# Kernel tuning notes

Hardware: AMD Instinct MI355X
Metric: run time of the kernel (lower is better)

The kernel has to match this reference:

```python
import jax, jax.numpy as jnp
import numpy as np

N_EMBED = 1024
HEAD_COUNT = 16
HEAD_SIZE = 64  # HEAD_COUNT * HEAD_SIZE == N_EMBED
SEQ = 2048
BATCH = 2


def setup_inputs() -> dict:
    key = jax.random.key(0)
    k_ix, k_q, k_k, k_v, k_p, k_b = jax.random.split(key, 6)
    scale = 1.0 / np.sqrt(N_EMBED)
    inp = {
        "ix": jax.random.normal(k_ix, (BATCH, SEQ, N_EMBED), dtype=jnp.float32),
        # per-head projection weights, stored as x @ W form: [H, C, D]
        "Wq": jax.random.normal(k_q, (HEAD_COUNT, N_EMBED, HEAD_SIZE), dtype=jnp.float32) * scale,
        "Wk": jax.random.normal(k_k, (HEAD_COUNT, N_EMBED, HEAD_SIZE), dtype=jnp.float32) * scale,
        "Wv": jax.random.normal(k_v, (HEAD_COUNT, N_EMBED, HEAD_SIZE), dtype=jnp.float32) * scale,
        # output projection (Linear with bias): y = x @ Wp + bp
        "Wp": jax.random.normal(k_p, (N_EMBED, N_EMBED), dtype=jnp.float32) * scale,
        "bp": jax.random.normal(k_b, (N_EMBED,), dtype=jnp.float32) * scale,
    }
    return inp


def reference(ix, Wq, Wk, Wv, Wp, bp):
    B, T, C = ix.shape
    # per-head projections: [B, H, T, D]
    Q = jnp.einsum("btc,hcd->bhtd", ix, Wq)
    K = jnp.einsum("btc,hcd->bhtd", ix, Wk)
    V = jnp.einsum("btc,hcd->bhtd", ix, Wv)
    # NOTE: faithful to source -- scores are MULTIPLIED by sqrt(C) (C = n_embed)
    scores = jnp.einsum("bhtd,bhsd->bhts", Q, K) * (C ** 0.5)
    causal = jnp.tril(jnp.ones((T, T), dtype=bool))
    scores = jnp.where(causal, scores, -jnp.inf)
    wei = jax.nn.softmax(scores, axis=-1)
    out = jnp.einsum("bhts,bhsd->bhtd", wei, V)
    # concat heads (matches torch.cat over per-head outputs along last dim)
    out = out.transpose(0, 2, 1, 3).reshape(B, T, -1)
    return out @ Wp + bp
```

## Files before the change

kernel.cpp:

```cpp
#include <hip/hip_runtime.h>

#define BATCH 2
#define SEQL  2048
#define NEMB  1024
#define NH    16
#define HD    64
#define MROWS (BATCH*SEQL)

#define QSCALE 46.166241308446828f

typedef short bf16x8 __attribute__((ext_vector_type(8)));
typedef float f32x16 __attribute__((ext_vector_type(16)));

__device__ __forceinline__ unsigned short f2bf(float x) {
    union { float f; unsigned u; } v; v.f = x;
    unsigned r = v.u + 0x7FFFu + ((v.u >> 16) & 1u);
    return (unsigned short)(r >> 16);
}
__device__ __forceinline__ void split_bf16(float x, unsigned short& hi, unsigned short& lo) {
    hi = f2bf(x);
    union { unsigned u; float f; } h; h.u = ((unsigned)hi) << 16;
    lo = f2bf(x - h.f);
}
__device__ __forceinline__ float bf2f(unsigned short b) {
    union { unsigned u; float f; } v; v.u = ((unsigned)b) << 16;
    return v.f;
}
__device__ __forceinline__ unsigned cvt_pk_bf16(float a, float b) {
    unsigned r;
    asm("v_cvt_pk_bf16_f32 %0, %1, %2" : "=v"(r) : "v"(a), "v"(b));
    return r;
}
__device__ __forceinline__ void plane_swap(unsigned& a, unsigned& b) {
    asm volatile("v_permlane32_swap_b32 %0, %1" : "+v"(a), "+v"(b));
}

__device__ __forceinline__ int slot16(int chunk, int lane) {
    return chunk * 66 + (lane & 31) + 33 * (lane >> 5);
}

__global__ __launch_bounds__(256) void convert_kernel(
    const float* __restrict__ ixsrc,
    const float* __restrict__ Wq, const float* __restrict__ Wk,
    const float* __restrict__ Wv, const float* __restrict__ Wp,
    unsigned short* __restrict__ ixhi, unsigned short* __restrict__ ixlo,
    unsigned short* __restrict__ qhi, unsigned short* __restrict__ qlo,
    unsigned short* __restrict__ khi, unsigned short* __restrict__ klo,
    unsigned short* __restrict__ vhi, unsigned short* __restrict__ pt)
{
    __shared__ float tile[64][68];
    const int bid = blockIdx.x;
    const int tid = threadIdx.x;

    if (bid < 4096) {
        int i = (bid * 256 + tid) * 4;
        float4 v = *(const float4*)(ixsrc + i);
        unsigned short h[4], l[4];
        split_bf16(v.x, h[0], l[0]); split_bf16(v.y, h[1], l[1]);
        split_bf16(v.z, h[2], l[2]); split_bf16(v.w, h[3], l[3]);
        uint2 ph, pl;
        ph.x = h[0] | ((unsigned)h[1] << 16); ph.y = h[2] | ((unsigned)h[3] << 16);
        pl.x = l[0] | ((unsigned)l[1] << 16); pl.y = l[2] | ((unsigned)l[3] << 16);
        *(uint2*)(ixhi + i) = ph;
        *(uint2*)(ixlo + i) = pl;
        return;
    }

    const int t  = bid - 4096;
    const int z  = t >> 8;
    const int rem = t & 255;
    const int hb = (rem >> 4) & 15;
    const int c0 = (rem & 15) * 64;
    const float* src; int rstride; unsigned short* dhi; unsigned short* dlo;
    if (z == 0)      { src = Wq + (size_t)hb * 65536; rstride = 64;   dhi = qhi; dlo = qlo; }
    else if (z == 1) { src = Wk + (size_t)hb * 65536; rstride = 64;   dhi = khi; dlo = klo; }
    else if (z == 2) { src = Wv + (size_t)hb * 65536; rstride = 64;   dhi = vhi; dlo = nullptr; }
    else             { src = Wp + (size_t)hb * 64;    rstride = 1024; dhi = pt;  dlo = nullptr; }
    #pragma unroll
    for (int i = 0; i < 4; ++i) {
        int fidx = i * 256 + tid;
        int r  = fidx >> 4;
        int dq = (fidx & 15) * 4;
        float4 v = *(const float4*)(src + (size_t)(c0 + r) * rstride + dq);
        *(float4*)&tile[r][dq] = v;
    }
    __syncthreads();
    #pragma unroll
    for (int i = 0; i < 4; ++i) {
        int fidx = i * 256 + tid;
        int d  = fidx >> 4;
        int cq = (fidx & 15) * 4;
        size_t base = (size_t)(hb * 64 + d) * 1024 + c0 + cq;
        unsigned short hh[4], ll[4];
        #pragma unroll
        for (int j = 0; j < 4; ++j) split_bf16(tile[cq + j][d], hh[j], ll[j]);
        uint2 ph; ph.x = hh[0] | ((unsigned)hh[1] << 16); ph.y = hh[2] | ((unsigned)hh[3] << 16);
        *(uint2*)(dhi + base) = ph;
        if (dlo) {
            uint2 pl; pl.x = ll[0] | ((unsigned)ll[1] << 16); pl.y = ll[2] | ((unsigned)ll[3] << 16);
            *(uint2*)(dlo + base) = pl;
        }
    }
}

__global__ __launch_bounds__(256, 2) void qkv_gemm(
    const unsigned short* __restrict__ Ahi, const unsigned short* __restrict__ Alo,
    const unsigned short* __restrict__ Bq_hi, const unsigned short* __restrict__ Bq_lo,
    const unsigned short* __restrict__ Bk_hi, const unsigned short* __restrict__ Bk_lo,
    const unsigned short* __restrict__ Bv_hi,
    unsigned short* __restrict__ Qhi, unsigned short* __restrict__ Qlo,
    unsigned short* __restrict__ Khi, unsigned short* __restrict__ Klo,
    unsigned short* __restrict__ Vt)
{
    __shared__ unsigned short smem[2][4][4224];

    const int bid = blockIdx.x;
    const int tid  = threadIdx.x;
    const int wid  = tid >> 6, lane = tid & 63;
    const int wr   = wid >> 1, wc = wid & 1;

    if (bid < 512) {
        const int z   = bid >> 8;
        const int xy  = bid & 255;
        const int m0  = (xy & 31) * 128;
        const int n0  = (xy >> 5) * 128;
        const unsigned short* __restrict__ Bhi = z ? Bk_hi : Bq_hi;
        const unsigned short* __restrict__ Blo = z ? Bk_lo : Bq_lo;
        unsigned short* __restrict__ Ohi = z ? Khi : Qhi;
        unsigned short* __restrict__ Olo = z ? Klo : Qlo;
        const float oscale = z ? 1.0f : QSCALE;

        int roff_[2], slot_[2];
        #pragma unroll
        for (int q = 0; q < 2; ++q) {
            int f   = q * 256 + tid;
            int row = f >> 2;
            int k8  = (f & 3) * 8;
            roff_[q] = row * 1024 + k8;
            slot_[q] = slot16((row >> 5) * 2 + (k8 >> 4), (row & 31) + 32 * ((k8 >> 3) & 1)) * 8;
        }
        const unsigned short* __restrict__ Ah = Ahi + (size_t)m0 * 1024;
        const unsigned short* __restrict__ Bh = Bhi + (size_t)n0 * 1024;
        const unsigned short* __restrict__ Al = Alo + (size_t)m0 * 1024;
        const unsigned short* __restrict__ Bl = Blo + (size_t)n0 * 1024;

        bf16x8 pah[2], pbh[2], pal[2], pbl[2];

        #define LOADT(KK)  do { _Pragma("unroll")                               \
            for (int q = 0; q < 2; ++q) {                                       \
                pah[q] = *(const bf16x8*)(Ah + roff_[q] + (KK));                \
                pbh[q] = *(const bf16x8*)(Bh + roff_[q] + (KK));                \
                pal[q] = *(const bf16x8*)(Al + roff_[q] + (KK));                \
                pbl[q] = *(const bf16x8*)(Bl + roff_[q] + (KK));                \
            } } while (0)

        #define WRITET(NB) do { _Pragma("unroll")                               \
            for (int q = 0; q < 2; ++q) {                                       \
                *(bf16x8*)(&smem[NB][0][slot_[q]]) = pah[q];                    \
                *(bf16x8*)(&smem[NB][1][slot_[q]]) = pbh[q];                    \
                *(bf16x8*)(&smem[NB][2][slot_[q]]) = pal[q];                    \
                *(bf16x8*)(&smem[NB][3][slot_[q]]) = pbl[q];                    \
            } } while (0)

        f32x16 acc[2][2] = {};

        LOADT(0);
        WRITET(0);
        LOADT(32);

        for (int t = 0; t < 32; ++t) {
            __syncthreads();
            if (t + 1 < 32) {
                WRITET((t + 1) & 1);
                if (t + 2 < 32) LOADT((t + 2) * 32);
            }
            const int cb = t & 1;
            const unsigned short* a_hi = smem[cb][0];
            const unsigned short* b_hi = smem[cb][1];
            const unsigned short* a_lo = smem[cb][2];
            const unsigned short* b_lo = smem[cb][3];

            #pragma unroll
            for (int kch = 0; kch < 2; ++kch) {
                bf16x8 ah[2], bh_[2], al[2], bl[2];
                #pragma unroll
                for (int mt = 0; mt < 2; ++mt) {
                    ah[mt] = *(const bf16x8*)(a_hi + slot16((2 * wr + mt) * 2 + kch, lane) * 8);
                    al[mt] = *(const bf16x8*)(a_lo + slot16((2 * wr + mt) * 2 + kch, lane) * 8);
                }
                #pragma unroll
                for (int nt = 0; nt < 2; ++nt) {
                    bh_[nt] = *(const bf16x8*)(b_hi + slot16((2 * wc + nt) * 2 + kch, lane) * 8);
                    bl[nt]  = *(const bf16x8*)(b_lo + slot16((2 * wc + nt) * 2 + kch, lane) * 8);
                }
                #pragma unroll
                for (int mt = 0; mt < 2; ++mt)
                    #pragma unroll
                    for (int nt = 0; nt < 2; ++nt) {
                        acc[mt][nt] = __builtin_amdgcn_mfma_f32_32x32x16_bf16(ah[mt], bh_[nt], acc[mt][nt], 0, 0, 0);
                        acc[mt][nt] = __builtin_amdgcn_mfma_f32_32x32x16_bf16(ah[mt], bl[nt],  acc[mt][nt], 0, 0, 0);
                        acc[mt][nt] = __builtin_amdgcn_mfma_f32_32x32x16_bf16(al[mt], bh_[nt], acc[mt][nt], 0, 0, 0);
                    }
            }
        }
        #undef LOADT
        #undef WRITET

        #pragma unroll
        for (int mt = 0; mt < 2; ++mt) {
            #pragma unroll
            for (int nt = 0; nt < 2; ++nt) {
                const int ncol = n0 + wc * 64 + nt * 32 + (lane & 31);
                const int head = ncol >> 6, d = ncol & 63;
                #pragma unroll
                for (int r = 0; r < 16; ++r) {
                    int mrow = m0 + wr * 64 + mt * 32 + (r & 3) + 8 * (r >> 2) + 4 * (lane >> 5);
                    int bb = mrow >> 11, tt = mrow & (SEQL - 1);
                    size_t idx = ((size_t)(bb * NH + head) * SEQL + tt) * HD + d;
                    float v = acc[mt][nt][r] * oscale;
                    unsigned short hi = f2bf(v);
                    Ohi[idx] = hi;
                    union { unsigned u; float f; } hf; hf.u = ((unsigned)hi) << 16;
                    Olo[idx] = f2bf(v - hf.f);
                }
            }
        }
    } else {
        const int vid = bid - 512;
        const int m0  = (vid >> 4) * 128;
        const int n0  = (vid & 15) * 64;

        int roffA_[2], slotA_[2], roffB, slotB;
        #pragma unroll
        for (int q = 0; q < 2; ++q) {
            int f   = q * 256 + tid;
            int row = f >> 2;
            int k8  = (f & 3) * 8;
            roffA_[q] = row * 1024 + k8;
            slotA_[q] = slot16((row >> 5) * 2 + (k8 >> 4), (row & 31) + 32 * ((k8 >> 3) & 1)) * 8;
        }
        {
            int row = tid >> 2;
            int k8  = (tid & 3) * 8;
            roffB  = row * 1024 + k8;
            slotB  = slot16((row >> 5) * 2 + (k8 >> 4), (row & 31) + 32 * ((k8 >> 3) & 1)) * 8;
        }
        const unsigned short* __restrict__ Ah = Ahi + (size_t)m0 * 1024;
        const unsigned short* __restrict__ Bh = Bv_hi + (size_t)n0 * 1024;

        bf16x8 pa[2], pb;
        #pragma unroll
        for (int q = 0; q < 2; ++q) pa[q] = *(const bf16x8*)(Ah + roffA_[q]);
        pb = *(const bf16x8*)(Bh + roffB);
        #pragma unroll
        for (int q = 0; q < 2; ++q) *(bf16x8*)(&smem[0][0][slotA_[q]]) = pa[q];
        *(bf16x8*)(&smem[0][1][slotB]) = pb;
        #pragma unroll
        for (int q = 0; q < 2; ++q) pa[q] = *(const bf16x8*)(Ah + roffA_[q] + 32);
        pb = *(const bf16x8*)(Bh + roffB + 32);

        f32x16 acc[2] = {};

        for (int t = 0; t < 32; ++t) {
            __syncthreads();
            if (t + 1 < 32) {
                const int nb = (t + 1) & 1;
                #pragma unroll
                for (int q = 0; q < 2; ++q) *(bf16x8*)(&smem[nb][0][slotA_[q]]) = pa[q];
                *(bf16x8*)(&smem[nb][1][slotB]) = pb;
                if (t + 2 < 32) {
                    #pragma unroll
                    for (int q = 0; q < 2; ++q) pa[q] = *(const bf16x8*)(Ah + roffA_[q] + (t + 2) * 32);
                    pb = *(const bf16x8*)(Bh + roffB + (t + 2) * 32);
                }
            }
            const int cb = t & 1;
            const unsigned short* a_s = smem[cb][0];
            const unsigned short* b_s = smem[cb][1];
            #pragma unroll
            for (int kch = 0; kch < 2; ++kch) {
                bf16x8 ah[2], bh_;
                #pragma unroll
                for (int mt = 0; mt < 2; ++mt)
                    ah[mt] = *(const bf16x8*)(a_s + slot16((2 * wr + mt) * 2 + kch, lane) * 8);
                bh_ = *(const bf16x8*)(b_s + slot16(wc * 2 + kch, lane) * 8);
                #pragma unroll
                for (int mt = 0; mt < 2; ++mt)
                    acc[mt] = __builtin_amdgcn_mfma_f32_32x32x16_bf16(bh_, ah[mt], acc[mt], 0, 0, 0);
            }
        }

        #pragma unroll
        for (int mt = 0; mt < 2; ++mt) {
            const int mcol = m0 + wr * 64 + mt * 32 + (lane & 31);
            const int bb = mcol >> 11, tt = mcol & (SEQL - 1);
            #pragma unroll
            for (int r = 0; r < 16; ++r) {
                int nrow = n0 + wc * 32 + (r & 3) + 8 * (r >> 2) + 4 * (lane >> 5);
                int head = nrow >> 6, dd = nrow & 63;
                Vt[((size_t)(bb * NH + head) * HD + dd) * SEQL + tt] = f2bf(acc[mt][r]);
            }
        }
    }
}

__global__ __launch_bounds__(256) void attn_mfma_kernel(
    const unsigned short* __restrict__ Qhi, const unsigned short* __restrict__ Qlo,
    const unsigned short* __restrict__ Khi, const unsigned short* __restrict__ Klo,
    const unsigned short* __restrict__ Vt,
    unsigned short* __restrict__ Op0, unsigned short* __restrict__ Op1,
    float* __restrict__ Ml)
{
    __shared__ unsigned short smem[2][3][4224];

    const int bid  = blockIdx.x;
    const int xcd  = bid & 7;
    const int idx  = bid >> 3;
    const int bh   = xcd * 4 + (idx & 3);
    const int rest = idx >> 2;
    const int j    = 15 - (rest >> 1);
    const int sp   = rest & 1;

    const int tid  = threadIdx.x;
    const int wid  = tid >> 6;
    const int lane = tid & 63;
    const int ln   = lane & 31;
    const int h    = lane >> 5;

    const int qb_idx = 4 * j + wid;
    const int qb     = qb_idx * 32;
    const int qglob  = qb + ln;
    const int cutoff = 2 * j + (wid >> 1);
    const int tbeg   = sp ? (j + 1) : 0;
    const int tend   = sp ? (2 * j + 2) : (j + 1);

    const unsigned short* __restrict__ Qbh = Qhi + (size_t)bh * SEQL * HD;
    const unsigned short* __restrict__ Qbl = Qlo + (size_t)bh * SEQL * HD;
    const unsigned short* __restrict__ Kbh = Khi + (size_t)bh * SEQL * HD;
    const unsigned short* __restrict__ Kbl = Klo + (size_t)bh * SEQL * HD;
    const unsigned short* __restrict__ Vtb = Vt  + (size_t)bh * HD * SEQL;

    bf16x8 qhi[4], qlo[4];
    #pragma unroll
    for (int c = 0; c < 4; ++c) {
        qhi[c] = *(const bf16x8*)(Qbh + (size_t)qglob * HD + c * 16 + h * 8);
        qlo[c] = *(const bf16x8*)(Qbl + (size_t)qglob * HD + c * 16 + h * 8);
    }

    int s_[2], d8_[2], ks_[2];
    #pragma unroll
    for (int ff = 0; ff < 2; ++ff) {
        int fidx = ff * 256 + tid;
        s_[ff]  = fidx >> 3;
        d8_[ff] = fidx & 7;
        ks_[ff] = slot16((s_[ff] >> 5) * 4 + (d8_[ff] >> 1),
                         (s_[ff] & 31) + 32 * (d8_[ff] & 1)) * 8;
    }

    bf16x8 kh[2], kl[2], vv[2];
    {
        const int s0p = tbeg * 64;
        #pragma unroll
        for (int ff = 0; ff < 2; ++ff) {
            kh[ff] = *(const bf16x8*)(Kbh + (size_t)(s0p + s_[ff]) * HD + d8_[ff] * 8);
            kl[ff] = *(const bf16x8*)(Kbl + (size_t)(s0p + s_[ff]) * HD + d8_[ff] * 8);
            vv[ff] = *(const bf16x8*)(Vtb + (size_t)s_[ff] * SEQL + s0p + d8_[ff] * 8);
        }
        const int pb = tbeg & 1;
        #pragma unroll
        for (int ff = 0; ff < 2; ++ff) {
            *(bf16x8*)(&smem[pb][0][ks_[ff]]) = kh[ff];
            *(bf16x8*)(&smem[pb][1][ks_[ff]]) = kl[ff];
            *(bf16x8*)(&smem[pb][2][ks_[ff]]) = vv[ff];
        }
        if (tbeg + 1 < tend) {
            const int s0n = (tbeg + 1) * 64;
            #pragma unroll
            for (int ff = 0; ff < 2; ++ff) {
                kh[ff] = *(const bf16x8*)(Kbh + (size_t)(s0n + s_[ff]) * HD + d8_[ff] * 8);
                kl[ff] = *(const bf16x8*)(Kbl + (size_t)(s0n + s_[ff]) * HD + d8_[ff] * 8);
                vv[ff] = *(const bf16x8*)(Vtb + (size_t)s_[ff] * SEQL + s0n + d8_[ff] * 8);
            }
        }
    }

    f32x16 oacc[2] = {};
    float m_run = -1e30f, l_run = 0.f;

    for (int t = tbeg; t < tend; ++t) {
        __syncthreads();
        if (t + 1 < tend) {
            const int nb = (t + 1) & 1;
            #pragma unroll
            for (int ff = 0; ff < 2; ++ff) {
                *(bf16x8*)(&smem[nb][0][ks_[ff]]) = kh[ff];
                *(bf16x8*)(&smem[nb][1][ks_[ff]]) = kl[ff];
                *(bf16x8*)(&smem[nb][2][ks_[ff]]) = vv[ff];
            }
            if (t + 2 < tend) {
                const int s0n = (t + 2) * 64;
                #pragma unroll
                for (int ff = 0; ff < 2; ++ff) {
                    kh[ff] = *(const bf16x8*)(Kbh + (size_t)(s0n + s_[ff]) * HD + d8_[ff] * 8);
                    kl[ff] = *(const bf16x8*)(Kbl + (size_t)(s0n + s_[ff]) * HD + d8_[ff] * 8);
                    vv[ff] = *(const bf16x8*)(Vtb + (size_t)s_[ff] * SEQL + s0n + d8_[ff] * 8);
                }
            }
        }

        if (t <= cutoff) {
            const int cb = t & 1;
            const int s0 = t * 64;
            const bf16x8* khf = (const bf16x8*)&smem[cb][0][0];
            const bf16x8* klf = (const bf16x8*)&smem[cb][1][0];
            const bf16x8* vtf = (const bf16x8*)&smem[cb][2][0];

            f32x16 sacc[2] = {};
            __builtin_amdgcn_s_setprio(1);
            #pragma unroll
            for (int sb = 0; sb < 2; ++sb) {
                #pragma unroll
                for (int c = 0; c < 4; ++c) {
                    bf16x8 ah = khf[slot16(sb * 4 + c, lane)];
                    bf16x8 al = klf[slot16(sb * 4 + c, lane)];
                    sacc[sb] = __builtin_amdgcn_mfma_f32_32x32x16_bf16(ah, qhi[c], sacc[sb], 0, 0, 0);
                    sacc[sb] = __builtin_amdgcn_mfma_f32_32x32x16_bf16(ah, qlo[c], sacc[sb], 0, 0, 0);
                    sacc[sb] = __builtin_amdgcn_mfma_f32_32x32x16_bf16(al, qhi[c], sacc[sb], 0, 0, 0);
                }
            }
            __builtin_amdgcn_s_setprio(0);

            if ((s0 + 63) > qb) {
                #pragma unroll
                for (int sb = 0; sb < 2; ++sb)
                    #pragma unroll
                    for (int r = 0; r < 16; ++r) {
                        int srow = (r & 3) + 8 * (r >> 2) + 4 * h + sb * 32;
                        if ((s0 + srow) > qglob) sacc[sb][r] = -1e30f;
                    }
            }

            float mtile = -1e30f;
            #pragma unroll
            for (int sb = 0; sb < 2; ++sb)
                #pragma unroll
                for (int r = 0; r < 16; ++r)
                    mtile = fmaxf(mtile, sacc[sb][r]);
            mtile = fmaxf(mtile, __shfl_xor(mtile, 32));

            if (!__all(mtile - m_run <= 11.5f)) {
                const float mnew  = fmaxf(m_run, mtile);
                const float alpha = exp2f(m_run - mnew);
                l_run *= alpha;
                #pragma unroll
                for (int dt = 0; dt < 2; ++dt)
                    #pragma unroll
                    for (int r = 0; r < 16; ++r)
                        oacc[dt][r] *= alpha;
                m_run = mnew;
            }

            float ps0 = 0.f, ps1 = 0.f;
            unsigned pw[2][8];
            #pragma unroll
            for (int sb = 0; sb < 2; ++sb) {
                #pragma unroll
                for (int r2 = 0; r2 < 8; ++r2) {
                    float p0 = exp2f(sacc[sb][2 * r2]     - m_run);
                    float p1 = exp2f(sacc[sb][2 * r2 + 1] - m_run);
                    if (sb == 0) ps0 += p0 + p1; else ps1 += p0 + p1;
                    pw[sb][r2] = cvt_pk_bf16(p0, p1);
                }
            }
            float psum = ps0 + ps1;
            psum += __shfl_xor(psum, 32);
            l_run += psum;

            bf16x8 pfrag[4];
            #pragma unroll
            for (int sb = 0; sb < 2; ++sb) {
                #pragma unroll
                for (int c = 0; c < 2; ++c) {
                    unsigned u0 = pw[sb][4 * c + 0], u2 = pw[sb][4 * c + 2];
                    unsigned u1 = pw[sb][4 * c + 1], u3 = pw[sb][4 * c + 3];
                    plane_swap(u0, u2);
                    plane_swap(u1, u3);
                    union { unsigned u[4]; bf16x8 v; } cvt;
                    cvt.u[0] = u0; cvt.u[1] = u1; cvt.u[2] = u2; cvt.u[3] = u3;
                    pfrag[sb * 2 + c] = cvt.v;
                }
            }

            __builtin_amdgcn_s_setprio(1);
            #pragma unroll
            for (int dt = 0; dt < 2; ++dt)
                #pragma unroll
                for (int sc = 0; sc < 4; ++sc)
                    oacc[dt] = __builtin_amdgcn_mfma_f32_32x32x16_bf16(
                        vtf[slot16(dt * 4 + sc, lane)], pfrag[sc], oacc[dt], 0, 0, 0);
            __builtin_amdgcn_s_setprio(0);
        }
    }

    unsigned short* op = (sp ? Op1 : Op0)
        + ((size_t)(bh >> 4) * SEQL + qglob) * NEMB + (bh & 15) * HD;
    #pragma unroll
    for (int dt = 0; dt < 2; ++dt) {
        #pragma unroll
        for (int rg = 0; rg < 4; ++rg) {
            int d0 = dt * 32 + rg * 8 + h * 4;
            uint2 w;
            w.x = cvt_pk_bf16(oacc[dt][rg * 4 + 0], oacc[dt][rg * 4 + 1]);
            w.y = cvt_pk_bf16(oacc[dt][rg * 4 + 2], oacc[dt][rg * 4 + 3]);
            *(uint2*)(op + d0) = w;
        }
    }
    if (h == 0) {
        float2 mlv; mlv.x = m_run; mlv.y = l_run;
        *(float2*)(Ml + ((size_t)(sp * 32 + bh) * SEQL + qglob) * 2) = mlv;
    }
}

__global__ __launch_bounds__(256) void attn_merge_kernel(
    unsigned short* __restrict__ Op0, const unsigned short* __restrict__ Op1,
    const float* __restrict__ Ml)
{
    const int gid  = blockIdx.x * 256 + threadIdx.x;
    const int row  = gid >> 7;
    const int col  = (gid & 127) * 8;
    const int bh   = ((row >> 11) << 4) + (col >> 6);
    const int q    = row & (SEQL - 1);

    float2 ml0 = *(const float2*)(Ml + ((size_t)bh * SEQL + q) * 2);
    float2 ml1 = *(const float2*)(Ml + ((size_t)(32 + bh) * SEQL + q) * 2);
    const float M  = fmaxf(ml0.x, ml1.x);
    const float w0 = exp2f(ml0.x - M);
    const float w1 = exp2f(ml1.x - M);
    const float rd = 1.0f / (ml0.y * w0 + ml1.y * w1);
    const float f0 = w0 * rd, f1 = w1 * rd;

    size_t off = (size_t)row * NEMB + col;
    uint4 a = *(const uint4*)(Op0 + off);
    uint4 b = *(const uint4*)(Op1 + off);
    const unsigned short* ap = (const unsigned short*)&a;
    const unsigned short* bp = (const unsigned short*)&b;
    uint4 o;
    unsigned* opw = (unsigned*)&o;
    #pragma unroll
    for (int i = 0; i < 4; ++i) {
        float r0 = bf2f(ap[2*i])     * f0 + bf2f(bp[2*i])     * f1;
        float r1 = bf2f(ap[2*i + 1]) * f0 + bf2f(bp[2*i + 1]) * f1;
        opw[i] = cvt_pk_bf16(r0, r1);
    }
    *(uint4*)(Op0 + off) = o;
}

__global__ __launch_bounds__(256, 2) void out_proj_kernel(
    const unsigned short* __restrict__ A, const unsigned short* __restrict__ B,
    const float* __restrict__ bias, float* __restrict__ out)
{
    __shared__ unsigned short smem[2][2][4224];

    const int m0 = blockIdx.x * 128;
    const int n0 = blockIdx.y * 128;
    const int tid  = threadIdx.x;
    const int wid  = tid >> 6, lane = tid & 63;
    const int wr   = wid >> 1, wc = wid & 1;

    int roff_[2], slot_[2];
    #pragma unroll
    for (int q = 0; q < 2; ++q) {
        int f   = q * 256 + tid;
        int row = f >> 2;
        int k8  = (f & 3) * 8;
        roff_[q] = row * 1024 + k8;
        slot_[q] = slot16((row >> 5) * 2 + (k8 >> 4), (row & 31) + 32 * ((k8 >> 3) & 1)) * 8;
    }
    const unsigned short* __restrict__ Ab = A + (size_t)m0 * 1024;
    const unsigned short* __restrict__ Bb = B + (size_t)n0 * 1024;

    bf16x8 pa[2], pb[2];
    #pragma unroll
    for (int q = 0; q < 2; ++q) {
        pa[q] = *(const bf16x8*)(Ab + roff_[q]);
        pb[q] = *(const bf16x8*)(Bb + roff_[q]);
    }
    #pragma unroll
    for (int q = 0; q < 2; ++q) {
        *(bf16x8*)(&smem[0][0][slot_[q]]) = pa[q];
        *(bf16x8*)(&smem[0][1][slot_[q]]) = pb[q];
    }
    #pragma unroll
    for (int q = 0; q < 2; ++q) {
        pa[q] = *(const bf16x8*)(Ab + roff_[q] + 32);
        pb[q] = *(const bf16x8*)(Bb + roff_[q] + 32);
    }

    f32x16 acc[2][2] = {};

    for (int t = 0; t < 32; ++t) {
        __syncthreads();
        if (t + 1 < 32) {
            const int nb = (t + 1) & 1;
            #pragma unroll
            for (int q = 0; q < 2; ++q) {
                *(bf16x8*)(&smem[nb][0][slot_[q]]) = pa[q];
                *(bf16x8*)(&smem[nb][1][slot_[q]]) = pb[q];
            }
            if (t + 2 < 32) {
                #pragma unroll
                for (int q = 0; q < 2; ++q) {
                    pa[q] = *(const bf16x8*)(Ab + roff_[q] + (t + 2) * 32);
                    pb[q] = *(const bf16x8*)(Bb + roff_[q] + (t + 2) * 32);
                }
            }
        }
        const int cb = t & 1;
        const unsigned short* a_s = smem[cb][0];
        const unsigned short* b_s = smem[cb][1];
        #pragma unroll
        for (int kch = 0; kch < 2; ++kch) {
            bf16x8 ah[2], bh_[2];
            #pragma unroll
            for (int mt = 0; mt < 2; ++mt)
                ah[mt] = *(const bf16x8*)(a_s + slot16((2 * wr + mt) * 2 + kch, lane) * 8);
            #pragma unroll
            for (int nt = 0; nt < 2; ++nt)
                bh_[nt] = *(const bf16x8*)(b_s + slot16((2 * wc + nt) * 2 + kch, lane) * 8);
            #pragma unroll
            for (int mt = 0; mt < 2; ++mt)
                #pragma unroll
                for (int nt = 0; nt < 2; ++nt)
                    acc[mt][nt] = __builtin_amdgcn_mfma_f32_32x32x16_bf16(ah[mt], bh_[nt], acc[mt][nt], 0, 0, 0);
        }
    }

    #pragma unroll
    for (int mt = 0; mt < 2; ++mt) {
        #pragma unroll
        for (int nt = 0; nt < 2; ++nt) {
            const int ncol = n0 + wc * 64 + nt * 32 + (lane & 31);
            const float bv = bias[ncol];
            #pragma unroll
            for (int r = 0; r < 16; ++r) {
                int mrow = m0 + wr * 64 + mt * 32 + (r & 3) + 8 * (r >> 2) + 4 * (lane >> 5);
                out[(size_t)mrow * 1024 + ncol] = acc[mt][nt][r] + bv;
            }
        }
    }
}

extern "C" void kernel_launch(void* const* d_in, const int* in_sizes, int n_in,
                              void* d_out, int out_size, void* d_ws, size_t ws_size,
                              hipStream_t stream)
{
    const float* ix = (const float*)d_in[0];
    const float* Wq = (const float*)d_in[1];
    const float* Wk = (const float*)d_in[2];
    const float* Wv = (const float*)d_in[3];
    const float* Wp = (const float*)d_in[4];
    const float* bp = (const float*)d_in[5];
    float* out = (float*)d_out;

    char* ws = (char*)d_ws;
    #define WSOFF(mb) ((unsigned short*)(ws + (size_t)(mb) * 1024 * 1024))
    unsigned short* ix_hi  = WSOFF(0);
    unsigned short* ix_lo  = WSOFF(8);
    unsigned short* Wqt_hi = WSOFF(16);
    unsigned short* Wqt_lo = WSOFF(18);
    unsigned short* Wkt_hi = WSOFF(20);
    unsigned short* Wkt_lo = WSOFF(22);
    unsigned short* Wvt_hi = WSOFF(24);
    unsigned short* Qhi    = WSOFF(26);
    unsigned short* Qlo    = WSOFF(34);
    unsigned short* Khi    = WSOFF(42);
    unsigned short* Klo    = WSOFF(50);
    unsigned short* Wpt    = WSOFF(58);
    unsigned short* Op0    = WSOFF(0);
    unsigned short* Op1    = WSOFF(8);
    float*          Ml     = (float*)WSOFF(16);
    unsigned short* Vt     = (unsigned short*)d_out;
    #undef WSOFF

    convert_kernel<<<5120, 256, 0, stream>>>(
        ix, Wq, Wk, Wv, Wp, ix_hi, ix_lo,
        Wqt_hi, Wqt_lo, Wkt_hi, Wkt_lo, Wvt_hi, Wpt);
    qkv_gemm<<<1024, 256, 0, stream>>>(
        ix_hi, ix_lo, Wqt_hi, Wqt_lo, Wkt_hi, Wkt_lo, Wvt_hi,
        Qhi, Qlo, Khi, Klo, Vt);
    attn_mfma_kernel<<<1024, 256, 0, stream>>>(Qhi, Qlo, Khi, Klo, Vt, Op0, Op1, Ml);
    attn_merge_kernel<<<MROWS * NEMB / 8 / 256, 256, 0, stream>>>(Op0, Op1, Ml);
    out_proj_kernel<<<dim3(MROWS / 128, NEMB / 128), 256, 0, stream>>>(Op0, Wpt, bp, out);
}
```

Measured before the change: 173.2 us.

## Fuse ix bf16 split into QKV GEMM and attention merge into out-proj

Removes the separate pass that converts ix into hi/lo bf16 planes. The QKV GEMM now loads fp32 ix directly and splits it to hi/lo bf16 in registers. The separate attention merge kernel is also removed. The out-projection kernel now reads both partial outputs plus their max/sum stats and combines them while loading its A tiles. This cuts two kernel launches and the intermediate global writes and reads, in exchange for double-width fp32 A loads and redundant conversion and merge arithmetic, since each A tile is reloaded by every N-block.

```diff
diff --git a/kernel.cpp b/kernel.cpp
--- a/kernel.cpp
+++ b/kernel.cpp
@@ -34,43 +34,38 @@
 __device__ __forceinline__ void plane_swap(unsigned& a, unsigned& b) {
     asm volatile("v_permlane32_swap_b32 %0, %1" : "+v"(a), "+v"(b));
 }
+__device__ __forceinline__ void split8(const float4& f0, const float4& f1,
+                                       bf16x8& hi8, bf16x8& lo8) {
+    const float* f = (const float*)&f0;
+    float tmp[8] = { f0.x, f0.y, f0.z, f0.w, f1.x, f1.y, f1.z, f1.w };
+    #pragma unroll
+    for (int j = 0; j < 8; ++j) {
+        unsigned short h, l;
+        split_bf16(tmp[j], h, l);
+        hi8[j] = (short)h;
+        lo8[j] = (short)l;
+    }
+    (void)f;
+}
 
 __device__ __forceinline__ int slot16(int chunk, int lane) {
     return chunk * 66 + (lane & 31) + 33 * (lane >> 5);
 }
 
 __global__ __launch_bounds__(256) void convert_kernel(
-    const float* __restrict__ ixsrc,
     const float* __restrict__ Wq, const float* __restrict__ Wk,
     const float* __restrict__ Wv, const float* __restrict__ Wp,
-    unsigned short* __restrict__ ixhi, unsigned short* __restrict__ ixlo,
     unsigned short* __restrict__ qhi, unsigned short* __restrict__ qlo,
     unsigned short* __restrict__ khi, unsigned short* __restrict__ klo,
     unsigned short* __restrict__ vhi, unsigned short* __restrict__ pt)
 {
     __shared__ float tile[64][68];
-    const int bid = blockIdx.x;
-    const int tid = threadIdx.x;
-
-    if (bid < 4096) {
-        int i = (bid * 256 + tid) * 4;
-        float4 v = *(const float4*)(ixsrc + i);
-        unsigned short h[4], l[4];
-        split_bf16(v.x, h[0], l[0]); split_bf16(v.y, h[1], l[1]);
-        split_bf16(v.z, h[2], l[2]); split_bf16(v.w, h[3], l[3]);
-        uint2 ph, pl;
-        ph.x = h[0] | ((unsigned)h[1] << 16); ph.y = h[2] | ((unsigned)h[3] << 16);
-        pl.x = l[0] | ((unsigned)l[1] << 16); pl.y = l[2] | ((unsigned)l[3] << 16);
-        *(uint2*)(ixhi + i) = ph;
-        *(uint2*)(ixlo + i) = pl;
-        return;
-    }
-
-    const int t  = bid - 4096;
+    const int t  = blockIdx.x;
     const int z  = t >> 8;
     const int rem = t & 255;
     const int hb = (rem >> 4) & 15;
     const int c0 = (rem & 15) * 64;
+    const int tid = threadIdx.x;
     const float* src; int rstride; unsigned short* dhi; unsigned short* dlo;
     if (z == 0)      { src = Wq + (size_t)hb * 65536; rstride = 64;   dhi = qhi; dlo = qlo; }
     else if (z == 1) { src = Wk + (size_t)hb * 65536; rstride = 64;   dhi = khi; dlo = klo; }
@@ -104,7 +99,7 @@
 }
 
 __global__ __launch_bounds__(256, 2) void qkv_gemm(
-    const unsigned short* __restrict__ Ahi, const unsigned short* __restrict__ Alo,
+    const float* __restrict__ ix,
     const unsigned short* __restrict__ Bq_hi, const unsigned short* __restrict__ Bq_lo,
     const unsigned short* __restrict__ Bk_hi, const unsigned short* __restrict__ Bk_lo,
     const unsigned short* __restrict__ Bv_hi,
@@ -139,18 +134,18 @@
             roff_[q] = row * 1024 + k8;
             slot_[q] = slot16((row >> 5) * 2 + (k8 >> 4), (row & 31) + 32 * ((k8 >> 3) & 1)) * 8;
         }
-        const unsigned short* __restrict__ Ah = Ahi + (size_t)m0 * 1024;
+        const float* __restrict__ Axf = ix + (size_t)m0 * 1024;
         const unsigned short* __restrict__ Bh = Bhi + (size_t)n0 * 1024;
-        const unsigned short* __restrict__ Al = Alo + (size_t)m0 * 1024;
         const unsigned short* __restrict__ Bl = Blo + (size_t)n0 * 1024;
 
         bf16x8 pah[2], pbh[2], pal[2], pbl[2];
 
         #define LOADT(KK)  do { _Pragma("unroll")                               \
             for (int q = 0; q < 2; ++q) {                                       \
-                pah[q] = *(const bf16x8*)(Ah + roff_[q] + (KK));                \
+                float4 f0 = *(const float4*)(Axf + roff_[q] + (KK));            \
+                float4 f1 = *(const float4*)(Axf + roff_[q] + (KK) + 4);        \
+                split8(f0, f1, pah[q], pal[q]);                                 \
                 pbh[q] = *(const bf16x8*)(Bh + roff_[q] + (KK));                \
-                pal[q] = *(const bf16x8*)(Al + roff_[q] + (KK));                \
                 pbl[q] = *(const bf16x8*)(Bl + roff_[q] + (KK));                \
             } } while (0)
 
@@ -245,18 +240,30 @@
             roffB  = row * 1024 + k8;
             slotB  = slot16((row >> 5) * 2 + (k8 >> 4), (row & 31) + 32 * ((k8 >> 3) & 1)) * 8;
         }
-        const unsigned short* __restrict__ Ah = Ahi + (size_t)m0 * 1024;
+        const float* __restrict__ Axf = ix + (size_t)m0 * 1024;
         const unsigned short* __restrict__ Bh = Bv_hi + (size_t)n0 * 1024;
 
         bf16x8 pa[2], pb;
         #pragma unroll
-        for (int q = 0; q < 2; ++q) pa[q] = *(const bf16x8*)(Ah + roffA_[q]);
+        for (int q = 0; q < 2; ++q) {
+            float4 f0 = *(const float4*)(Axf + roffA_[q]);
+            float4 f1 = *(const float4*)(Axf + roffA_[q] + 4);
+            float t8[8] = { f0.x, f0.y, f0.z, f0.w, f1.x, f1.y, f1.z, f1.w };
+            #pragma unroll
+            for (int j = 0; j < 8; ++j) pa[q][j] = (short)f2bf(t8[j]);
+        }
         pb = *(const bf16x8*)(Bh + roffB);
         #pragma unroll
         for (int q = 0; q < 2; ++q) *(bf16x8*)(&smem[0][0][slotA_[q]]) = pa[q];
         *(bf16x8*)(&smem[0][1][slotB]) = pb;
         #pragma unroll
-        for (int q = 0; q < 2; ++q) pa[q] = *(const bf16x8*)(Ah + roffA_[q] + 32);
+        for (int q = 0; q < 2; ++q) {
+            float4 f0 = *(const float4*)(Axf + roffA_[q] + 32);
+            float4 f1 = *(const float4*)(Axf + roffA_[q] + 36);
+            float t8[8] = { f0.x, f0.y, f0.z, f0.w, f1.x, f1.y, f1.z, f1.w };
+            #pragma unroll
+            for (int j = 0; j < 8; ++j) pa[q][j] = (short)f2bf(t8[j]);
+        }
         pb = *(const bf16x8*)(Bh + roffB + 32);
 
         f32x16 acc[2] = {};
@@ -270,7 +277,13 @@
                 *(bf16x8*)(&smem[nb][1][slotB]) = pb;
                 if (t + 2 < 32) {
                     #pragma unroll
-                    for (int q = 0; q < 2; ++q) pa[q] = *(const bf16x8*)(Ah + roffA_[q] + (t + 2) * 32);
+                    for (int q = 0; q < 2; ++q) {
+                        float4 f0 = *(const float4*)(Axf + roffA_[q] + (t + 2) * 32);
+                        float4 f1 = *(const float4*)(Axf + roffA_[q] + (t + 2) * 32 + 4);
+                        float t8[8] = { f0.x, f0.y, f0.z, f0.w, f1.x, f1.y, f1.z, f1.w };
+                        #pragma unroll
+                        for (int j = 0; j < 8; ++j) pa[q][j] = (short)f2bf(t8[j]);
+                    }
                     pb = *(const bf16x8*)(Bh + roffB + (t + 2) * 32);
                 }
             }
@@ -521,42 +534,10 @@
     }
 }
 
-__global__ __launch_bounds__(256) void attn_merge_kernel(
-    unsigned short* __restrict__ Op0, const unsigned short* __restrict__ Op1,
-    const float* __restrict__ Ml)
-{
-    const int gid  = blockIdx.x * 256 + threadIdx.x;
-    const int row  = gid >> 7;
-    const int col  = (gid & 127) * 8;
-    const int bh   = ((row >> 11) << 4) + (col >> 6);
-    const int q    = row & (SEQL - 1);
-
-    float2 ml0 = *(const float2*)(Ml + ((size_t)bh * SEQL + q) * 2);
-    float2 ml1 = *(const float2*)(Ml + ((size_t)(32 + bh) * SEQL + q) * 2);
-    const float M  = fmaxf(ml0.x, ml1.x);
-    const float w0 = exp2f(ml0.x - M);
-    const float w1 = exp2f(ml1.x - M);
-    const float rd = 1.0f / (ml0.y * w0 + ml1.y * w1);
-    const float f0 = w0 * rd, f1 = w1 * rd;
-
-    size_t off = (size_t)row * NEMB + col;
-    uint4 a = *(const uint4*)(Op0 + off);
-    uint4 b = *(const uint4*)(Op1 + off);
-    const unsigned short* ap = (const unsigned short*)&a;
-    const unsigned short* bp = (const unsigned short*)&b;
-    uint4 o;
-    unsigned* opw = (unsigned*)&o;
-    #pragma unroll
-    for (int i = 0; i < 4; ++i) {
-        float r0 = bf2f(ap[2*i])     * f0 + bf2f(bp[2*i])     * f1;
-        float r1 = bf2f(ap[2*i + 1]) * f0 + bf2f(bp[2*i + 1]) * f1;
-        opw[i] = cvt_pk_bf16(r0, r1);
-    }
-    *(uint4*)(Op0 + off) = o;
-}
-
 __global__ __launch_bounds__(256, 2) void out_proj_kernel(
-    const unsigned short* __restrict__ A, const unsigned short* __restrict__ B,
+    const unsigned short* __restrict__ Op0, const unsigned short* __restrict__ Op1,
+    const float* __restrict__ Ml,
+    const unsigned short* __restrict__ B,
     const float* __restrict__ bias, float* __restrict__ out)
 {
     __shared__ unsigned short smem[2][2][4224];
@@ -567,22 +548,49 @@
     const int wid  = tid >> 6, lane = tid & 63;
     const int wr   = wid >> 1, wc = wid & 1;
 
-    int roff_[2], slot_[2];
+    int roff_[2], slot_[2], k8_[2];
+    size_t mlbase_[2];
     #pragma unroll
     for (int q = 0; q < 2; ++q) {
         int f   = q * 256 + tid;
         int row = f >> 2;
         int k8  = (f & 3) * 8;
         roff_[q] = row * 1024 + k8;
+        k8_[q]   = k8;
         slot_[q] = slot16((row >> 5) * 2 + (k8 >> 4), (row & 31) + 32 * ((k8 >> 3) & 1)) * 8;
-    }
-    const unsigned short* __restrict__ Ab = A + (size_t)m0 * 1024;
+        const int mrow = m0 + row;
+        mlbase_[q] = ((size_t)(mrow >> 11) * 16 * SEQL + (mrow & (SEQL - 1))) * 2;
+    }
+    const size_t abase = (size_t)m0 * 1024;
     const unsigned short* __restrict__ Bb = B + (size_t)n0 * 1024;
 
+    #define LOADA(q, KK, dst) do {                                              \
+        const int col  = (KK) + k8_[q];                                         \
+        const int head = col >> 6;                                              \
+        const size_t mloff = mlbase_[q] + (size_t)head * (SEQL * 2);            \
+        float2 ml0 = *(const float2*)(Ml + mloff);                              \
+        float2 ml1 = *(const float2*)(Ml + mloff + 32 * SEQL * 2);              \
+        const float M  = fmaxf(ml0.x, ml1.x);                                   \
+        const float w0 = exp2f(ml0.x - M);                                      \
+        const float w1 = exp2f(ml1.x - M);                                      \
+        const float rd = 1.0f / (ml0.y * w0 + ml1.y * w1);                      \
+        const float f0 = w0 * rd, f1 = w1 * rd;                                 \
+        uint4 av = *(const uint4*)(Op0 + abase + roff_[q] + (KK));              \
+        uint4 bv = *(const uint4*)(Op1 + abase + roff_[q] + (KK));              \
+        const unsigned short* ap = (const unsigned short*)&av;                  \
+        const unsigned short* bp = (const unsigned short*)&bv;                  \
+        unsigned* dw = (unsigned*)&(dst);                                       \
+        _Pragma("unroll")                                                       \
+        for (int i_ = 0; i_ < 4; ++i_) {                                        \
+            float r0 = bf2f(ap[2*i_])   * f0 + bf2f(bp[2*i_])   * f1;           \
+            float r1 = bf2f(ap[2*i_+1]) * f0 + bf2f(bp[2*i_+1]) * f1;           \
+            dw[i_] = cvt_pk_bf16(r0, r1);                                       \
+        } } while (0)
+
     bf16x8 pa[2], pb[2];
     #pragma unroll
     for (int q = 0; q < 2; ++q) {
-        pa[q] = *(const bf16x8*)(Ab + roff_[q]);
+        LOADA(q, 0, pa[q]);
         pb[q] = *(const bf16x8*)(Bb + roff_[q]);
     }
     #pragma unroll
@@ -592,7 +600,7 @@
     }
     #pragma unroll
     for (int q = 0; q < 2; ++q) {
-        pa[q] = *(const bf16x8*)(Ab + roff_[q] + 32);
+        LOADA(q, 32, pa[q]);
         pb[q] = *(const bf16x8*)(Bb + roff_[q] + 32);
     }
 
@@ -610,7 +618,7 @@
             if (t + 2 < 32) {
                 #pragma unroll
                 for (int q = 0; q < 2; ++q) {
-                    pa[q] = *(const bf16x8*)(Ab + roff_[q] + (t + 2) * 32);
+                    LOADA(q, (t + 2) * 32, pa[q]);
                     pb[q] = *(const bf16x8*)(Bb + roff_[q] + (t + 2) * 32);
                 }
             }
@@ -634,6 +642,7 @@
                     acc[mt][nt] = __builtin_amdgcn_mfma_f32_32x32x16_bf16(ah[mt], bh_[nt], acc[mt][nt], 0, 0, 0);
         }
     }
+    #undef LOADA
 
     #pragma unroll
     for (int mt = 0; mt < 2; ++mt) {
@@ -664,8 +673,6 @@
 
     char* ws = (char*)d_ws;
     #define WSOFF(mb) ((unsigned short*)(ws + (size_t)(mb) * 1024 * 1024))
-    unsigned short* ix_hi  = WSOFF(0);
-    unsigned short* ix_lo  = WSOFF(8);
     unsigned short* Wqt_hi = WSOFF(16);
     unsigned short* Wqt_lo = WSOFF(18);
     unsigned short* Wkt_hi = WSOFF(20);
@@ -682,13 +689,12 @@
     unsigned short* Vt     = (unsigned short*)d_out;
     #undef WSOFF
 
-    convert_kernel<<<5120, 256, 0, stream>>>(
-        ix, Wq, Wk, Wv, Wp, ix_hi, ix_lo,
-        Wqt_hi, Wqt_lo, Wkt_hi, Wkt_lo, Wvt_hi, Wpt);
+    convert_kernel<<<1024, 256, 0, stream>>>(
+        Wq, Wk, Wv, Wp, Wqt_hi, Wqt_lo, Wkt_hi, Wkt_lo, Wvt_hi, Wpt);
     qkv_gemm<<<1024, 256, 0, stream>>>(
-        ix_hi, ix_lo, Wqt_hi, Wqt_lo, Wkt_hi, Wkt_lo, Wvt_hi,
+        ix, Wqt_hi, Wqt_lo, Wkt_hi, Wkt_lo, Wvt_hi,
         Qhi, Qlo, Khi, Klo, Vt);
     attn_mfma_kernel<<<1024, 256, 0, stream>>>(Qhi, Qlo, Khi, Klo, Vt, Op0, Op1, Ml);
-    attn_merge_kernel<<<MROWS * NEMB / 8 / 256, 256, 0, stream>>>(Op0, Op1, Ml);
-    out_proj_kernel<<<dim3(MROWS / 128, NEMB / 128), 256, 0, stream>>>(Op0, Wpt, bp, out);
-}
+    out_proj_kernel<<<dim3(MROWS / 128, NEMB / 128), 256, 0, stream>>>(
+        Op0, Op1, Ml, Wpt, bp, out);
+}
```

After: 189.3 us. 9.3% more time.

## Stage Q/K projection GEMM tiles via direct global-to-LDS loads

Applied to the files above, without the earlier changes.

The Q/K branch of the QKV projection kernel now copies its hi/lo A and B tiles straight from global memory into LDS with global_load_lds (16-byte lanes), instead of loading into registers and then writing to LDS. The shared layout becomes unpadded and fragment-major, so each wave's load lands exactly where the MFMA fragment reads expect it. The V branch is updated to index the flattened buffer. The aim is to cut VGPR staging, LDS write instructions and register pressure, and to overlap the next tile's fetch with MFMA work. In exchange it drops the padded bank-conflict-avoiding layout and relies on correct vmcnt waits before the barrier.

```diff
diff --git a/kernel.cpp b/kernel.cpp
--- a/kernel.cpp
+++ b/kernel.cpp
@@ -33,6 +33,9 @@
 }
 __device__ __forceinline__ void plane_swap(unsigned& a, unsigned& b) {
     asm volatile("v_permlane32_swap_b32 %0, %1" : "+v"(a), "+v"(b));
+}
+__device__ __forceinline__ void gload_lds16(const unsigned short* g, unsigned short* l) {
+    __builtin_amdgcn_global_load_lds((const unsigned int*)g, (unsigned int*)l, 16, 0, 0);
 }
 
 __device__ __forceinline__ int slot16(int chunk, int lane) {
@@ -112,7 +115,7 @@
     unsigned short* __restrict__ Khi, unsigned short* __restrict__ Klo,
     unsigned short* __restrict__ Vt)
 {
-    __shared__ unsigned short smem[2][4][4224];
+    __shared__ unsigned short smem[32768];
 
     const int bid = blockIdx.x;
     const int tid  = threadIdx.x;
@@ -130,68 +133,54 @@
         unsigned short* __restrict__ Olo = z ? Klo : Qlo;
         const float oscale = z ? 1.0f : QSCALE;
 
-        int roff_[2], slot_[2];
-        #pragma unroll
-        for (int q = 0; q < 2; ++q) {
-            int f   = q * 256 + tid;
-            int row = f >> 2;
-            int k8  = (f & 3) * 8;
-            roff_[q] = row * 1024 + k8;
-            slot_[q] = slot16((row >> 5) * 2 + (k8 >> 4), (row & 31) + 32 * ((k8 >> 3) & 1)) * 8;
-        }
         const unsigned short* __restrict__ Ah = Ahi + (size_t)m0 * 1024;
         const unsigned short* __restrict__ Bh = Bhi + (size_t)n0 * 1024;
         const unsigned short* __restrict__ Al = Alo + (size_t)m0 * 1024;
         const unsigned short* __restrict__ Bl = Blo + (size_t)n0 * 1024;
 
-        bf16x8 pah[2], pbh[2], pal[2], pbl[2];
-
-        #define LOADT(KK)  do { _Pragma("unroll")                               \
-            for (int q = 0; q < 2; ++q) {                                       \
-                pah[q] = *(const bf16x8*)(Ah + roff_[q] + (KK));                \
-                pbh[q] = *(const bf16x8*)(Bh + roff_[q] + (KK));                \
-                pal[q] = *(const bf16x8*)(Al + roff_[q] + (KK));                \
-                pbl[q] = *(const bf16x8*)(Bl + roff_[q] + (KK));                \
-            } } while (0)
-
-        #define WRITET(NB) do { _Pragma("unroll")                               \
-            for (int q = 0; q < 2; ++q) {                                       \
-                *(bf16x8*)(&smem[NB][0][slot_[q]]) = pah[q];                    \
-                *(bf16x8*)(&smem[NB][1][slot_[q]]) = pbh[q];                    \
-                *(bf16x8*)(&smem[NB][2][slot_[q]]) = pal[q];                    \
-                *(bf16x8*)(&smem[NB][3][slot_[q]]) = pbl[q];                    \
-            } } while (0)
+        const size_t goff = (size_t)(wid * 32 + (lane & 31)) * 1024 + (lane >> 5) * 8;
+        const int cb0 = wid * 2 * 512;
+
+        #define ISSUE(KK, NB) do {                                              \
+            unsigned short* lb = smem + (NB) * 16384 + cb0;                     \
+            gload_lds16(Ah + goff + (KK),      lb + 0 * 4096);                  \
+            gload_lds16(Ah + goff + (KK) + 16, lb + 0 * 4096 + 512);            \
+            gload_lds16(Bh + goff + (KK),      lb + 1 * 4096);                  \
+            gload_lds16(Bh + goff + (KK) + 16, lb + 1 * 4096 + 512);            \
+            gload_lds16(Al + goff + (KK),      lb + 2 * 4096);                  \
+            gload_lds16(Al + goff + (KK) + 16, lb + 2 * 4096 + 512);            \
+            gload_lds16(Bl + goff + (KK),      lb + 3 * 4096);                  \
+            gload_lds16(Bl + goff + (KK) + 16, lb + 3 * 4096 + 512);            \
+        } while (0)
 
         f32x16 acc[2][2] = {};
 
-        LOADT(0);
-        WRITET(0);
-        LOADT(32);
+        ISSUE(0, 0);
 
         for (int t = 0; t < 32; ++t) {
             __syncthreads();
-            if (t + 1 < 32) {
-                WRITET((t + 1) & 1);
-                if (t + 2 < 32) LOADT((t + 2) * 32);
-            }
-            const int cb = t & 1;
-            const unsigned short* a_hi = smem[cb][0];
-            const unsigned short* b_hi = smem[cb][1];
-            const unsigned short* a_lo = smem[cb][2];
-            const unsigned short* b_lo = smem[cb][3];
+            if (t + 1 < 32) ISSUE((t + 1) * 32, (t + 1) & 1);
+
+            const unsigned short* base = smem + (t & 1) * 16384;
+            const unsigned short* a_hi = base;
+            const unsigned short* b_hi = base + 4096;
+            const unsigned short* a_lo = base + 8192;
+            const unsigned short* b_lo = base + 12288;
 
             #pragma unroll
             for (int kch = 0; kch < 2; ++kch) {
                 bf16x8 ah[2], bh_[2], al[2], bl[2];
                 #pragma unroll
                 for (int mt = 0; mt < 2; ++mt) {
-                    ah[mt] = *(const bf16x8*)(a_hi + slot16((2 * wr + mt) * 2 + kch, lane) * 8);
-                    al[mt] = *(const bf16x8*)(a_lo + slot16((2 * wr + mt) * 2 + kch, lane) * 8);
+                    const int off = (((2 * wr + mt) * 2 + kch) * 64 + lane) * 8;
+                    ah[mt] = *(const bf16x8*)(a_hi + off);
+                    al[mt] = *(const bf16x8*)(a_lo + off);
                 }
                 #pragma unroll
                 for (int nt = 0; nt < 2; ++nt) {
-                    bh_[nt] = *(const bf16x8*)(b_hi + slot16((2 * wc + nt) * 2 + kch, lane) * 8);
-                    bl[nt]  = *(const bf16x8*)(b_lo + slot16((2 * wc + nt) * 2 + kch, lane) * 8);
+                    const int off = (((2 * wc + nt) * 2 + kch) * 64 + lane) * 8;
+                    bh_[nt] = *(const bf16x8*)(b_hi + off);
+                    bl[nt]  = *(const bf16x8*)(b_lo + off);
                 }
                 #pragma unroll
                 for (int mt = 0; mt < 2; ++mt)
@@ -203,8 +192,7 @@
                     }
             }
         }
-        #undef LOADT
-        #undef WRITET
+        #undef ISSUE
 
         #pragma unroll
         for (int mt = 0; mt < 2; ++mt) {
@@ -253,8 +241,8 @@
         for (int q = 0; q < 2; ++q) pa[q] = *(const bf16x8*)(Ah + roffA_[q]);
         pb = *(const bf16x8*)(Bh + roffB);
         #pragma unroll
-        for (int q = 0; q < 2; ++q) *(bf16x8*)(&smem[0][0][slotA_[q]]) = pa[q];
-        *(bf16x8*)(&smem[0][1][slotB]) = pb;
+        for (int q = 0; q < 2; ++q) *(bf16x8*)(smem + slotA_[q]) = pa[q];
+        *(bf16x8*)(smem + 8192 + slotB) = pb;
         #pragma unroll
         for (int q = 0; q < 2; ++q) pa[q] = *(const bf16x8*)(Ah + roffA_[q] + 32);
         pb = *(const bf16x8*)(Bh + roffB + 32);
@@ -266,17 +254,16 @@
             if (t + 1 < 32) {
                 const int nb = (t + 1) & 1;
                 #pragma unroll
-                for (int q = 0; q < 2; ++q) *(bf16x8*)(&smem[nb][0][slotA_[q]]) = pa[q];
-                *(bf16x8*)(&smem[nb][1][slotB]) = pb;
+                for (int q = 0; q < 2; ++q) *(bf16x8*)(smem + nb * 16384 + slotA_[q]) = pa[q];
+                *(bf16x8*)(smem + nb * 16384 + 8192 + slotB) = pb;
                 if (t + 2 < 32) {
                     #pragma unroll
                     for (int q = 0; q < 2; ++q) pa[q] = *(const bf16x8*)(Ah + roffA_[q] + (t + 2) * 32);
                     pb = *(const bf16x8*)(Bh + roffB + (t + 2) * 32);
                 }
             }
-            const int cb = t & 1;
-            const unsigned short* a_s = smem[cb][0];
-            const unsigned short* b_s = smem[cb][1];
+            const unsigned short* a_s = smem + (t & 1) * 16384;
+            const unsigned short* b_s = a_s + 8192;
             #pragma unroll
             for (int kch = 0; kch < 2; ++kch) {
                 bf16x8 ah[2], bh_;
```

Result: no change. 176.6 us (+2.0%).
